# Kernel tuning notes

Hardware: AMD Instinct MI355X
Metric: run time of the kernel (lower is better)

Reference implementation:

```python
import jax, jax.numpy as jnp
import numpy as np

EMBED_DIM = 1024
NUM_HEADS = 16
HEAD_DIM = EMBED_DIM // NUM_HEADS


def setup_inputs() -> dict:
    key = jax.random.key(0)
    ks = jax.random.split(key, 9)
    B, S, E = 2, 2048, EMBED_DIM
    scale = 1.0 / np.sqrt(E)
    x = jax.random.normal(ks[0], (B, S, E), dtype=jnp.float32)
    Wq = jax.random.normal(ks[1], (E, E), dtype=jnp.float32) * scale
    bq = jax.random.normal(ks[2], (E,), dtype=jnp.float32) * 0.01
    Wk = jax.random.normal(ks[3], (E, E), dtype=jnp.float32) * scale
    bk = jax.random.normal(ks[4], (E,), dtype=jnp.float32) * 0.01
    Wv = jax.random.normal(ks[5], (E, E), dtype=jnp.float32) * scale
    bv = jax.random.normal(ks[6], (E,), dtype=jnp.float32) * 0.01
    Wo = jax.random.normal(ks[7], (E, E), dtype=jnp.float32) * scale
    bo = jax.random.normal(ks[8], (E,), dtype=jnp.float32) * 0.01
    return {"x": x, "Wq": Wq, "bq": bq, "Wk": Wk, "bk": bk,
            "Wv": Wv, "bv": bv, "Wo": Wo, "bo": bo}


def reference(x, Wq, bq, Wk, bk, Wv, bv, Wo, bo):
    B, S, E = x.shape
    H, D = NUM_HEADS, HEAD_DIM
    # projections (torch Linear: x @ W.T + b), reshape to (B, H, S, D)
    q = (x @ Wq.T + bq).reshape(B, S, H, D).transpose(0, 2, 1, 3)
    k = (x @ Wk.T + bk).reshape(B, S, H, D).transpose(0, 2, 1, 3)
    v = (x @ Wv.T + bv).reshape(B, S, H, D).transpose(0, 2, 1, 3)
    softmax_scale = 1.0 / np.sqrt(D)
    # (B, H, S, S) scores, causal mask, stable softmax
    scores = softmax_scale * jnp.einsum('bhsd,bhtd->bhst', q, k)
    causal = jnp.tril(jnp.ones((S, S), dtype=bool))  # True = keep
    scores = jnp.where(causal, scores, -jnp.inf)
    attn = jax.nn.softmax(scores, axis=-1)
    out = jnp.einsum('bhst,bhtd->bhsd', attn, v)  # (B, H, S, D)
    out = out.transpose(0, 2, 1, 3).reshape(B, S, E)
    return out @ Wo.T + bo
```

## Files before the change

kernel.cpp:

```cpp
#include <hip/hip_runtime.h>
#include <cstdint>
#include <cstddef>

#define SEQ   2048
#define BATCH 2
#define EMB   1024
#define NH    16
#define HD    64
#define MTOT  (BATCH * SEQ)
#define NX    (MTOT * EMB)
#define NW    (EMB * EMB)

typedef __bf16 bf16_t;
typedef __bf16 bf16x2 __attribute__((ext_vector_type(2)));
typedef __bf16 bf16x4 __attribute__((ext_vector_type(4)));
typedef __bf16 bf16x8 __attribute__((ext_vector_type(8)));
typedef float  f32x4  __attribute__((ext_vector_type(4)));
typedef float  f32x16 __attribute__((ext_vector_type(16)));

typedef __attribute__((address_space(1))) const void* as1cv;
typedef __attribute__((address_space(3))) void*       as3v;

__device__ __forceinline__ void async_cp16(const void* g, void* l) {
  __builtin_amdgcn_global_load_lds((as1cv)g, (as3v)l, 16, 0, 0);
}

__device__ __forceinline__ f32x4 mfma16(bf16x8 a, bf16x8 b, f32x4 c) {
  return __builtin_amdgcn_mfma_f32_16x16x32_bf16(a, b, c, 0, 0, 0);
}
__device__ __forceinline__ f32x16 mfma32(bf16x8 a, bf16x8 b, f32x16 c) {
  return __builtin_amdgcn_mfma_f32_32x32x16_bf16(a, b, c, 0, 0, 0);
}

__device__ __forceinline__ uint32_t pk2(float a, float b) {
  bf16x2 t; t[0] = (bf16_t)a; t[1] = (bf16_t)b;
  return __builtin_bit_cast(uint32_t, t);
}
__device__ __forceinline__ bf16x8 mk_frag(uint32_t x, uint32_t y,
                                          uint32_t z, uint32_t w) {
  uint4 u; u.x = x; u.y = y; u.z = z; u.w = w;
  return __builtin_bit_cast(bf16x8, u);
}

__global__ __launch_bounds__(256) void cvt_all(
    const float* __restrict__ x,  const float* __restrict__ wq,
    const float* __restrict__ wk, const float* __restrict__ wv,
    const float* __restrict__ wo,
    bf16_t* __restrict__ xb,  bf16_t* __restrict__ wqb,
    bf16_t* __restrict__ wkb, bf16_t* __restrict__ wvb,
    bf16_t* __restrict__ wob) {
  long e = ((long)blockIdx.x * 256 + threadIdx.x) * 4;
  const float* s; bf16_t* d; long off;
  if (e < NX) { s = x; d = xb; off = e; }
  else {
    long e2 = e - NX;
    int w = (int)(e2 >> 20);
    off = e2 & (NW - 1);
    s = (w == 0) ? wq : (w == 1) ? wk : (w == 2) ? wv : wo;
    d = (w == 0) ? wqb : (w == 1) ? wkb : (w == 2) ? wvb : wob;
  }
  float4 v = *(const float4*)(s + off);
  bf16x4 o;
  o[0] = (bf16_t)v.x; o[1] = (bf16_t)v.y; o[2] = (bf16_t)v.z; o[3] = (bf16_t)v.w;
  *(bf16x4*)(d + off) = o;
}

__global__ __launch_bounds__(256) void vtrans(const bf16_t* __restrict__ V,
                                              bf16_t* __restrict__ VT) {
  const int hb = blockIdx.x;
  const int sb = blockIdx.y;
  const int h = hb & 15, b = hb >> 4;
  const int t = threadIdx.x;
  __shared__ __align__(16) bf16_t Ts[64 * 72];
  const bf16_t* Vp = V + ((size_t)(b * SEQ + sb * 64)) * EMB + h * HD;
  const int sr = t >> 4, d0 = (t & 15) * 4;
#pragma unroll
  for (int i = 0; i < 4; ++i) {
    bf16x4 v = *(const bf16x4*)(Vp + (size_t)(sr + 16 * i) * EMB + d0);
    *(bf16x4*)&Ts[(sr + 16 * i) * 72 + d0] = v;
  }
  __syncthreads();
  const int d = t >> 2, tc = (t & 3) * 16;
  __align__(16) bf16_t out[16];
#pragma unroll
  for (int j = 0; j < 16; ++j) out[j] = Ts[(tc + j) * 72 + d];
  bf16_t* dst = VT + ((size_t)hb * HD + d) * SEQ + sb * 64 + tc;
  *(uint4*)(dst)     = *(uint4*)&out[0];
  *(uint4*)(dst + 8) = *(uint4*)&out[8];
}

template <typename OT>
__global__ __launch_bounds__(256) void gemm_bt3(
    const bf16_t* __restrict__ A,
    const bf16_t* __restrict__ W0, const bf16_t* __restrict__ W1,
    const bf16_t* __restrict__ W2,
    const float* __restrict__ b0, const float* __restrict__ b1,
    const float* __restrict__ b2,
    OT* __restrict__ C0, OT* __restrict__ C1, OT* __restrict__ C2) {
  constexpr int K = EMB, N = EMB, BK = 64;
  const int z = blockIdx.z;
  const bf16_t* B    = (z == 0) ? W0 : (z == 1) ? W1 : W2;
  const float*  bias = (z == 0) ? b0 : (z == 1) ? b1 : b2;
  OT*           C    = (z == 0) ? C0 : (z == 1) ? C1 : C2;

  __shared__ __align__(16) bf16_t As[128 * BK];
  __shared__ __align__(16) bf16_t Bs[64 * BK];

  const int tid  = threadIdx.x;
  const int lane = tid & 63;
  const int wave = tid >> 6;
  const int quad = lane >> 4;
  const int l16  = lane & 15;
  const int wm   = wave * 32;
  const int m0   = blockIdx.y * 128;
  const int n0   = blockIdx.x * 64;

  const int row0 = tid >> 3;
  const int slot = tid & 7;
  const bf16_t* gA[4];
  const bf16_t* gB[2];
#pragma unroll
  for (int i = 0; i < 4; ++i) {
    const int r = row0 + 32 * i;
    gA[i] = A + (size_t)(m0 + r) * K + (slot ^ (r & 7)) * 8;
  }
#pragma unroll
  for (int i = 0; i < 2; ++i) {
    const int r = row0 + 32 * i;
    gB[i] = B + (size_t)(n0 + r) * K + (slot ^ (r & 7)) * 8;
  }

  f32x4 acc[2][4] = {};
  const int sw = l16 & 7;

  for (int kk = 0; kk < K; kk += BK) {
#pragma unroll
    for (int i = 0; i < 4; ++i)
      async_cp16(gA[i] + kk, &As[(tid + 256 * i) * 8]);
#pragma unroll
    for (int i = 0; i < 2; ++i)
      async_cp16(gB[i] + kk, &Bs[(tid + 256 * i) * 8]);
    __syncthreads();

    bf16x8 af[2][2], bfr[2][4];
#pragma unroll
    for (int ks = 0; ks < 2; ++ks) {
      const int js = ((ks * 4 + quad) ^ sw) * 8;
#pragma unroll
      for (int i = 0; i < 2; ++i)
        af[ks][i] = *(const bf16x8*)&As[(wm + i * 16 + l16) * BK + js];
#pragma unroll
      for (int j = 0; j < 4; ++j)
        bfr[ks][j] = *(const bf16x8*)&Bs[(j * 16 + l16) * BK + js];
    }
#pragma unroll
    for (int ks = 0; ks < 2; ++ks)
#pragma unroll
      for (int i = 0; i < 2; ++i)
#pragma unroll
        for (int j = 0; j < 4; ++j)
          acc[i][j] = mfma16(af[ks][i], bfr[ks][j], acc[i][j]);
    __syncthreads();
  }

#pragma unroll
  for (int j = 0; j < 4; ++j) {
    const int col = n0 + j * 16 + l16;
    const float bv = bias[col];
#pragma unroll
    for (int i = 0; i < 2; ++i) {
      const int row = m0 + wm + i * 16 + quad * 4;
#pragma unroll
      for (int r = 0; r < 4; ++r) {
        C[(size_t)(row + r) * N + col] = (OT)(acc[i][j][r] + bv);
      }
    }
  }
}

__global__ __launch_bounds__(256, 3) void attn128(
    const bf16_t* __restrict__ Qg, const bf16_t* __restrict__ Kg,
    const bf16_t* __restrict__ VTg, bf16_t* __restrict__ Og) {
  const int hb  = blockIdx.x;
  const int y   = blockIdx.y;
  const int s   = (y < 8) ? (15 - y) : (y - 8);
  const int h   = hb & 15, b = hb >> 4;
  const int tid = threadIdx.x;
  const int lane = tid & 63, wave = tid >> 6;
  const int l31 = lane & 31, hi = lane >> 5;
  const bool h0 = (hi == 0);

  __shared__ __align__(16) bf16_t Ks[2][64 * 72];
  __shared__ __align__(16) bf16_t VsT[2][64 * 72];
  __shared__ __align__(16) bf16_t Qs[128 * 64];

  const size_t base = ((size_t)b * SEQ) * EMB + (size_t)h * HD;
  const bf16_t* Kp  = Kg + base;
  const bf16_t* VTp = VTg + (size_t)hb * HD * SEQ;

  const int kr0r = tid >> 3, kcol = (tid & 7) * 8;
  const int kr1r = kr0r + 32;
  const int lo0 = kr0r * 72 + kcol;
  const int lo1 = lo0 + 32 * 72;

  const int q0  = s * 128;
  const int nit = 2 * s + 2;
  const bf16_t* Qp = Qg + base + (size_t)q0 * EMB;

  uint4 kr0 = *(const uint4*)(Kp + (size_t)kr0r * EMB + kcol);
  uint4 kr1 = *(const uint4*)(Kp + (size_t)kr1r * EMB + kcol);
  uint4 vr0 = *(const uint4*)(VTp + (size_t)kr0r * SEQ + kcol);
  uint4 vr1 = *(const uint4*)(VTp + (size_t)kr1r * SEQ + kcol);

#pragma unroll
  for (int i = 0; i < 4; ++i) {
    const int c = tid + 256 * i;
    *(uint4*)&Qs[(c >> 3) * 64 + (c & 7) * 8] =
        *(const uint4*)(Qp + (size_t)(c >> 3) * EMB + (c & 7) * 8);
  }
  __syncthreads();

  bf16x8 qf[4];
#pragma unroll
  for (int kk = 0; kk < 4; ++kk)
    qf[kk] = *(const bf16x8*)&Qs[(32 * wave + l31) * 64 + kk * 16 + hi * 8];

  f32x16 acc_t0 = {}, acc_t1 = {};
  float lsum = 0.f;

  for (int it = 0; it < nit; ++it) {
    bf16_t* Kc = &Ks[it & 1][0];
    bf16_t* Vc = &VsT[it & 1][0];
    *(uint4*)&Kc[lo0] = kr0;
    *(uint4*)&Kc[lo1] = kr1;
    *(uint4*)&Vc[lo0] = vr0;
    *(uint4*)&Vc[lo1] = vr1;
    __syncthreads();

    if (it + 1 < nit) {
      const bf16_t* Kn  = Kp + (size_t)(it + 1) * 64 * EMB;
      const bf16_t* VTn = VTp + (it + 1) * 64;
      kr0 = *(const uint4*)(Kn + (size_t)kr0r * EMB + kcol);
      kr1 = *(const uint4*)(Kn + (size_t)kr1r * EMB + kcol);
      vr0 = *(const uint4*)(VTn + (size_t)kr0r * SEQ + kcol);
      vr1 = *(const uint4*)(VTn + (size_t)kr1r * SEQ + kcol);
    }

    const bool active = (64 * it <= q0 + 32 * wave + 31);
    if (active) {
      f32x16 s0 = {}, s1 = {};
#pragma unroll
      for (int kk = 0; kk < 4; ++kk) {
        const bf16x8 kf0 = *(const bf16x8*)&Kc[l31 * 72 + kk * 16 + hi * 8];
        const bf16x8 kf1 =
            *(const bf16x8*)&Kc[(32 + l31) * 72 + kk * 16 + hi * 8];
        s0 = mfma32(kf0, qf[kk], s0);
        s1 = mfma32(kf1, qf[kk], s1);
      }

      constexpr float SC2 = 0.18033688011112042f;
      if (it >= nit - 2) {
        const int qg = q0 + 32 * wave + l31;
        const int k0 = 64 * it + 4 * hi;
#pragma unroll
        for (int r = 0; r < 16; ++r) {
          const int key = k0 + (r & 3) + 8 * (r >> 2);
          float p0 = exp2f(__builtin_fmaf(s0[r], SC2, -8.f));
          float p1 = exp2f(__builtin_fmaf(s1[r], SC2, -8.f));
          if (key > qg) p0 = 0.f;
          if (key + 32 > qg) p1 = 0.f;
          s0[r] = p0; s1[r] = p1;
          lsum += p0 + p1;
        }
      } else {
#pragma unroll
        for (int r = 0; r < 16; ++r) {
          const float p0 = exp2f(__builtin_fmaf(s0[r], SC2, -8.f));
          const float p1 = exp2f(__builtin_fmaf(s1[r], SC2, -8.f));
          s0[r] = p0; s1[r] = p1;
          lsum += p0 + p1;
        }
      }

      bf16x8 pf[4];
#pragma unroll
      for (int kk = 0; kk < 4; ++kk) {
        const f32x16& g = (kk < 2) ? s0 : s1;
        const int bir = 8 * (kk & 1);
        const uint32_t PL0 = pk2(g[bir + 0], g[bir + 1]);
        const uint32_t PL1 = pk2(g[bir + 2], g[bir + 3]);
        const uint32_t PH0 = pk2(g[bir + 4], g[bir + 5]);
        const uint32_t PH1 = pk2(g[bir + 6], g[bir + 7]);
        const uint32_t XL0 = (uint32_t)__shfl_xor((int)PL0, 32, 64);
        const uint32_t XL1 = (uint32_t)__shfl_xor((int)PL1, 32, 64);
        const uint32_t XH0 = (uint32_t)__shfl_xor((int)PH0, 32, 64);
        const uint32_t XH1 = (uint32_t)__shfl_xor((int)PH1, 32, 64);
        pf[kk] = h0 ? mk_frag(PL0, PL1, XL0, XL1)
                    : mk_frag(XH0, XH1, PH0, PH1);
      }

#pragma unroll
      for (int kk = 0; kk < 4; ++kk) {
        const bf16x8 vf0 = *(const bf16x8*)&Vc[l31 * 72 + kk * 16 + hi * 8];
        const bf16x8 vf1 =
            *(const bf16x8*)&Vc[(32 + l31) * 72 + kk * 16 + hi * 8];
        acc_t0 = mfma32(vf0, pf[kk], acc_t0);
        acc_t1 = mfma32(vf1, pf[kk], acc_t1);
      }
    }
  }

  const float lt = lsum + __shfl_xor(lsum, 32, 64);
  const float inv = 1.f / lt;
  bf16_t* Ow = &Qs[(32 * wave) * 64];
#pragma unroll
  for (int a = 0; a < 4; ++a)
#pragma unroll
    for (int c = 0; c < 4; c += 2) {
      const int r = 4 * a + c;
      const int d = c + 8 * a + 4 * hi;
      *(uint32_t*)&Ow[l31 * 64 + d] =
          pk2(acc_t0[r] * inv, acc_t0[r + 1] * inv);
      *(uint32_t*)&Ow[l31 * 64 + d + 32] =
          pk2(acc_t1[r] * inv, acc_t1[r + 1] * inv);
    }
  bf16_t* Op = Og + base + (size_t)(q0 + 32 * wave) * EMB;
#pragma unroll
  for (int i = 0; i < 4; ++i) {
    const int id = lane + 64 * i;
    const int row = id >> 3, col8 = (id & 7) * 8;
    *(uint4*)(Op + (size_t)row * EMB + col8) =
        *(const uint4*)&Ow[row * 64 + col8];
  }
}

extern "C" void kernel_launch(void* const* d_in, const int* in_sizes, int n_in,
                              void* d_out, int out_size, void* d_ws,
                              size_t ws_size, hipStream_t stream) {
  const float* x  = (const float*)d_in[0];
  const float* Wq = (const float*)d_in[1];
  const float* bq = (const float*)d_in[2];
  const float* Wk = (const float*)d_in[3];
  const float* bk = (const float*)d_in[4];
  const float* Wv = (const float*)d_in[5];
  const float* bv = (const float*)d_in[6];
  const float* Wo = (const float*)d_in[7];
  const float* bo = (const float*)d_in[8];
  float* out = (float*)d_out;

  char* p = (char*)d_ws;
  bf16_t* xb  = (bf16_t*)p; p += (size_t)NX * 2;
  bf16_t* wqb = (bf16_t*)p; p += (size_t)NW * 2;
  bf16_t* wkb = (bf16_t*)p; p += (size_t)NW * 2;
  bf16_t* wvb = (bf16_t*)p; p += (size_t)NW * 2;
  bf16_t* wob = (bf16_t*)p; p += (size_t)NW * 2;
  bf16_t* qb  = (bf16_t*)p; p += (size_t)NX * 2;
  bf16_t* kb  = (bf16_t*)p; p += (size_t)NX * 2;
  bf16_t* vb  = (bf16_t*)p; p += (size_t)NX * 2;
  bf16_t* ab  = (bf16_t*)p; p += (size_t)NX * 2;
  bf16_t* vtb = xb;

  const int ntot = NX + 4 * NW;
  cvt_all<<<dim3(ntot / 4 / 256), 256, 0, stream>>>(
      x, Wq, Wk, Wv, Wo, xb, wqb, wkb, wvb, wob);

  gemm_bt3<bf16_t><<<dim3(EMB / 64, MTOT / 128, 3), 256, 0, stream>>>(
      xb, wqb, wkb, wvb, bq, bk, bv, qb, kb, vb);

  vtrans<<<dim3(BATCH * NH, SEQ / 64), 256, 0, stream>>>(vb, vtb);

  attn128<<<dim3(BATCH * NH, SEQ / 128), 256, 0, stream>>>(qb, kb, vtb, ab);

  gemm_bt3<float><<<dim3(EMB / 64, MTOT / 128, 1), 256, 0, stream>>>(
      ab, wob, wob, wob, bo, bo, bo, out, out, out);
}
```

Measured before the change: 191.6 us.

## Fuse QKV projection into one wide GEMM with 32x32 MFMA tiles

```diff
diff --git a/kernel.cpp b/kernel.cpp
--- a/kernel.cpp
+++ b/kernel.cpp
@@ -10,6 +10,7 @@
 #define MTOT  (BATCH * SEQ)
 #define NX    (MTOT * EMB)
 #define NW    (EMB * EMB)
+#define QS    3072
 
 typedef __bf16 bf16_t;
 typedef __bf16 bf16x2 __attribute__((ext_vector_type(2)));
@@ -25,9 +26,6 @@
   __builtin_amdgcn_global_load_lds((as1cv)g, (as3v)l, 16, 0, 0);
 }
 
-__device__ __forceinline__ f32x4 mfma16(bf16x8 a, bf16x8 b, f32x4 c) {
-  return __builtin_amdgcn_mfma_f32_16x16x32_bf16(a, b, c, 0, 0, 0);
-}
 __device__ __forceinline__ f32x16 mfma32(bf16x8 a, bf16x8 b, f32x16 c) {
   return __builtin_amdgcn_mfma_f32_32x32x16_bf16(a, b, c, 0, 0, 0);
 }
@@ -65,18 +63,18 @@
   *(bf16x4*)(d + off) = o;
 }
 
-__global__ __launch_bounds__(256) void vtrans(const bf16_t* __restrict__ V,
+__global__ __launch_bounds__(256) void vtrans(const bf16_t* __restrict__ QKV,
                                               bf16_t* __restrict__ VT) {
   const int hb = blockIdx.x;
   const int sb = blockIdx.y;
   const int h = hb & 15, b = hb >> 4;
   const int t = threadIdx.x;
   __shared__ __align__(16) bf16_t Ts[64 * 72];
-  const bf16_t* Vp = V + ((size_t)(b * SEQ + sb * 64)) * EMB + h * HD;
+  const bf16_t* Vp = QKV + ((size_t)(b * SEQ + sb * 64)) * QS + 2048 + h * HD;
   const int sr = t >> 4, d0 = (t & 15) * 4;
 #pragma unroll
   for (int i = 0; i < 4; ++i) {
-    bf16x4 v = *(const bf16x4*)(Vp + (size_t)(sr + 16 * i) * EMB + d0);
+    bf16x4 v = *(const bf16x4*)(Vp + (size_t)(sr + 16 * i) * QS + d0);
     *(bf16x4*)&Ts[(sr + 16 * i) * 72 + d0] = v;
   }
   __syncthreads();
@@ -89,98 +87,85 @@
   *(uint4*)(dst + 8) = *(uint4*)&out[8];
 }
 
-template <typename OT>
-__global__ __launch_bounds__(256) void gemm_bt3(
-    const bf16_t* __restrict__ A,
-    const bf16_t* __restrict__ W0, const bf16_t* __restrict__ W1,
-    const bf16_t* __restrict__ W2,
+template <typename OT, int BN, int CS>
+__global__ __launch_bounds__(256) void gemm_f(
+    const bf16_t* __restrict__ A, const bf16_t* __restrict__ Bw,
     const float* __restrict__ b0, const float* __restrict__ b1,
-    const float* __restrict__ b2,
-    OT* __restrict__ C0, OT* __restrict__ C1, OT* __restrict__ C2) {
-  constexpr int K = EMB, N = EMB, BK = 64;
-  const int z = blockIdx.z;
-  const bf16_t* B    = (z == 0) ? W0 : (z == 1) ? W1 : W2;
-  const float*  bias = (z == 0) ? b0 : (z == 1) ? b1 : b2;
-  OT*           C    = (z == 0) ? C0 : (z == 1) ? C1 : C2;
-
+    const float* __restrict__ b2, OT* __restrict__ C) {
+  constexpr int K = EMB, BK = 64;
   __shared__ __align__(16) bf16_t As[128 * BK];
-  __shared__ __align__(16) bf16_t Bs[64 * BK];
+  __shared__ __align__(16) bf16_t Bs[BN * BK];
 
   const int tid  = threadIdx.x;
   const int lane = tid & 63;
   const int wave = tid >> 6;
-  const int quad = lane >> 4;
-  const int l16  = lane & 15;
-  const int wm   = wave * 32;
+  const int l31  = lane & 31;
+  const int hi   = lane >> 5;
+  const int wm   = (wave >> 1) * 64;
+  const int wn   = (wave & 1) * (BN / 2);
   const int m0   = blockIdx.y * 128;
-  const int n0   = blockIdx.x * 64;
-
-  const int row0 = tid >> 3;
-  const int slot = tid & 7;
+  const int n0   = blockIdx.x * BN;
+
+  const float* bias = (n0 < 1024) ? b0 : ((n0 < 2048) ? b1 : b2);
+
+  const int row0 = tid >> 3, slot = tid & 7;
   const bf16_t* gA[4];
-  const bf16_t* gB[2];
-#pragma unroll
-  for (int i = 0; i < 4; ++i) {
-    const int r = row0 + 32 * i;
-    gA[i] = A + (size_t)(m0 + r) * K + (slot ^ (r & 7)) * 8;
-  }
-#pragma unroll
-  for (int i = 0; i < 2; ++i) {
-    const int r = row0 + 32 * i;
-    gB[i] = B + (size_t)(n0 + r) * K + (slot ^ (r & 7)) * 8;
-  }
-
-  f32x4 acc[2][4] = {};
-  const int sw = l16 & 7;
+  const bf16_t* gB[BN / 32];
+#pragma unroll
+  for (int i = 0; i < 4; ++i)
+    gA[i] = A + (size_t)(m0 + row0 + 32 * i) * K + (slot ^ (row0 & 7)) * 8;
+#pragma unroll
+  for (int i = 0; i < BN / 32; ++i)
+    gB[i] = Bw + (size_t)(n0 + row0 + 32 * i) * K + (slot ^ (row0 & 7)) * 8;
+
+  f32x16 acc[2][BN / 64] = {};
+  const int sw = l31 & 7;
 
   for (int kk = 0; kk < K; kk += BK) {
 #pragma unroll
     for (int i = 0; i < 4; ++i)
       async_cp16(gA[i] + kk, &As[(tid + 256 * i) * 8]);
 #pragma unroll
-    for (int i = 0; i < 2; ++i)
+    for (int i = 0; i < BN / 32; ++i)
       async_cp16(gB[i] + kk, &Bs[(tid + 256 * i) * 8]);
     __syncthreads();
 
-    bf16x8 af[2][2], bfr[2][4];
-#pragma unroll
-    for (int ks = 0; ks < 2; ++ks) {
-      const int js = ((ks * 4 + quad) ^ sw) * 8;
+#pragma unroll
+    for (int ks = 0; ks < 4; ++ks) {
+      const int js = ((ks * 2 + hi) ^ sw) * 8;
+      bf16x8 af[2], bfr[BN / 64];
 #pragma unroll
       for (int i = 0; i < 2; ++i)
-        af[ks][i] = *(const bf16x8*)&As[(wm + i * 16 + l16) * BK + js];
-#pragma unroll
-      for (int j = 0; j < 4; ++j)
-        bfr[ks][j] = *(const bf16x8*)&Bs[(j * 16 + l16) * BK + js];
-    }
-#pragma unroll
-    for (int ks = 0; ks < 2; ++ks)
+        af[i] = *(const bf16x8*)&As[(wm + i * 32 + l31) * BK + js];
+#pragma unroll
+      for (int j = 0; j < BN / 64; ++j)
+        bfr[j] = *(const bf16x8*)&Bs[(wn + j * 32 + l31) * BK + js];
 #pragma unroll
       for (int i = 0; i < 2; ++i)
 #pragma unroll
-        for (int j = 0; j < 4; ++j)
-          acc[i][j] = mfma16(af[ks][i], bfr[ks][j], acc[i][j]);
+        for (int j = 0; j < BN / 64; ++j)
+          acc[i][j] = mfma32(af[i], bfr[j], acc[i][j]);
+    }
     __syncthreads();
   }
 
 #pragma unroll
-  for (int j = 0; j < 4; ++j) {
-    const int col = n0 + j * 16 + l16;
-    const float bv = bias[col];
-#pragma unroll
-    for (int i = 0; i < 2; ++i) {
-      const int row = m0 + wm + i * 16 + quad * 4;
-#pragma unroll
-      for (int r = 0; r < 4; ++r) {
-        C[(size_t)(row + r) * N + col] = (OT)(acc[i][j][r] + bv);
-      }
-    }
-  }
+  for (int i = 0; i < 2; ++i)
+#pragma unroll
+    for (int j = 0; j < BN / 64; ++j) {
+      const int col = n0 + wn + j * 32 + l31;
+      const float bv = bias[col & 1023];
+#pragma unroll
+      for (int r = 0; r < 16; ++r) {
+        const int row = m0 + wm + i * 32 + (r & 3) + 8 * (r >> 2) + 4 * hi;
+        C[(size_t)row * CS + col] = (OT)(acc[i][j][r] + bv);
+      }
+    }
 }
 
 __global__ __launch_bounds__(256, 3) void attn128(
-    const bf16_t* __restrict__ Qg, const bf16_t* __restrict__ Kg,
-    const bf16_t* __restrict__ VTg, bf16_t* __restrict__ Og) {
+    const bf16_t* __restrict__ QKVg, const bf16_t* __restrict__ VTg,
+    bf16_t* __restrict__ Og) {
   const int hb  = blockIdx.x;
   const int y   = blockIdx.y;
   const int s   = (y < 8) ? (15 - y) : (y - 8);
@@ -194,8 +179,9 @@
   __shared__ __align__(16) bf16_t VsT[2][64 * 72];
   __shared__ __align__(16) bf16_t Qs[128 * 64];
 
-  const size_t base = ((size_t)b * SEQ) * EMB + (size_t)h * HD;
-  const bf16_t* Kp  = Kg + base;
+  const size_t base = ((size_t)b * SEQ) * QS + (size_t)h * HD;
+  const bf16_t* Qb  = QKVg + base;
+  const bf16_t* Kp  = QKVg + base + 1024;
   const bf16_t* VTp = VTg + (size_t)hb * HD * SEQ;
 
   const int kr0r = tid >> 3, kcol = (tid & 7) * 8;
@@ -205,10 +191,10 @@
 
   const int q0  = s * 128;
   const int nit = 2 * s + 2;
-  const bf16_t* Qp = Qg + base + (size_t)q0 * EMB;
-
-  uint4 kr0 = *(const uint4*)(Kp + (size_t)kr0r * EMB + kcol);
-  uint4 kr1 = *(const uint4*)(Kp + (size_t)kr1r * EMB + kcol);
+  const bf16_t* Qp = Qb + (size_t)q0 * QS;
+
+  uint4 kr0 = *(const uint4*)(Kp + (size_t)kr0r * QS + kcol);
+  uint4 kr1 = *(const uint4*)(Kp + (size_t)kr1r * QS + kcol);
   uint4 vr0 = *(const uint4*)(VTp + (size_t)kr0r * SEQ + kcol);
   uint4 vr1 = *(const uint4*)(VTp + (size_t)kr1r * SEQ + kcol);
 
@@ -216,7 +202,7 @@
   for (int i = 0; i < 4; ++i) {
     const int c = tid + 256 * i;
     *(uint4*)&Qs[(c >> 3) * 64 + (c & 7) * 8] =
-        *(const uint4*)(Qp + (size_t)(c >> 3) * EMB + (c & 7) * 8);
+        *(const uint4*)(Qp + (size_t)(c >> 3) * QS + (c & 7) * 8);
   }
   __syncthreads();
 
@@ -238,10 +224,10 @@
     __syncthreads();
 
     if (it + 1 < nit) {
-      const bf16_t* Kn  = Kp + (size_t)(it + 1) * 64 * EMB;
+      const bf16_t* Kn  = Kp + (size_t)(it + 1) * 64 * QS;
       const bf16_t* VTn = VTp + (it + 1) * 64;
-      kr0 = *(const uint4*)(Kn + (size_t)kr0r * EMB + kcol);
-      kr1 = *(const uint4*)(Kn + (size_t)kr1r * EMB + kcol);
+      kr0 = *(const uint4*)(Kn + (size_t)kr0r * QS + kcol);
+      kr1 = *(const uint4*)(Kn + (size_t)kr1r * QS + kcol);
       vr0 = *(const uint4*)(VTn + (size_t)kr0r * SEQ + kcol);
       vr1 = *(const uint4*)(VTn + (size_t)kr1r * SEQ + kcol);
     }
@@ -324,7 +310,7 @@
       *(uint32_t*)&Ow[l31 * 64 + d + 32] =
           pk2(acc_t1[r] * inv, acc_t1[r + 1] * inv);
     }
-  bf16_t* Op = Og + base + (size_t)(q0 + 32 * wave) * EMB;
+  bf16_t* Op = Og + ((size_t)b * SEQ + q0 + 32 * wave) * EMB + (size_t)h * HD;
 #pragma unroll
   for (int i = 0; i < 4; ++i) {
     const int id = lane + 64 * i;
@@ -349,28 +335,26 @@
   float* out = (float*)d_out;
 
   char* p = (char*)d_ws;
-  bf16_t* xb  = (bf16_t*)p; p += (size_t)NX * 2;
-  bf16_t* wqb = (bf16_t*)p; p += (size_t)NW * 2;
-  bf16_t* wkb = (bf16_t*)p; p += (size_t)NW * 2;
-  bf16_t* wvb = (bf16_t*)p; p += (size_t)NW * 2;
-  bf16_t* wob = (bf16_t*)p; p += (size_t)NW * 2;
-  bf16_t* qb  = (bf16_t*)p; p += (size_t)NX * 2;
-  bf16_t* kb  = (bf16_t*)p; p += (size_t)NX * 2;
-  bf16_t* vb  = (bf16_t*)p; p += (size_t)NX * 2;
-  bf16_t* ab  = (bf16_t*)p; p += (size_t)NX * 2;
-  bf16_t* vtb = xb;
+  bf16_t* xb   = (bf16_t*)p; p += (size_t)NX * 2;
+  bf16_t* wqb  = (bf16_t*)p; p += (size_t)NW * 2;
+  bf16_t* wkb  = (bf16_t*)p; p += (size_t)NW * 2;
+  bf16_t* wvb  = (bf16_t*)p; p += (size_t)NW * 2;
+  bf16_t* wob  = (bf16_t*)p; p += (size_t)NW * 2;
+  bf16_t* qkvb = (bf16_t*)p; p += (size_t)NX * 3 * 2;
+  bf16_t* ab   = (bf16_t*)p; p += (size_t)NX * 2;
+  bf16_t* vtb  = xb;
 
   const int ntot = NX + 4 * NW;
   cvt_all<<<dim3(ntot / 4 / 256), 256, 0, stream>>>(
       x, Wq, Wk, Wv, Wo, xb, wqb, wkb, wvb, wob);
 
-  gemm_bt3<bf16_t><<<dim3(EMB / 64, MTOT / 128, 3), 256, 0, stream>>>(
-      xb, wqb, wkb, wvb, bq, bk, bv, qb, kb, vb);
-
-  vtrans<<<dim3(BATCH * NH, SEQ / 64), 256, 0, stream>>>(vb, vtb);
-
-  attn128<<<dim3(BATCH * NH, SEQ / 128), 256, 0, stream>>>(qb, kb, vtb, ab);
-
-  gemm_bt3<float><<<dim3(EMB / 64, MTOT / 128, 1), 256, 0, stream>>>(
-      ab, wob, wob, wob, bo, bo, bo, out, out, out);
-}
+  gemm_f<bf16_t, 128, QS><<<dim3(QS / 128, MTOT / 128), 256, 0, stream>>>(
+      xb, wqb, bq, bk, bv, qkvb);
+
+  vtrans<<<dim3(BATCH * NH, SEQ / 64), 256, 0, stream>>>(qkvb, vtb);
+
+  attn128<<<dim3(BATCH * NH, SEQ / 128), 256, 0, stream>>>(qkvb, vtb, ab);
+
+  gemm_f<float, 64, EMB><<<dim3(EMB / 64, MTOT / 128), 256, 0, stream>>>(
+      ab, wob, bo, bo, bo, out);
+}
```

After: 187.4 us. 2.2% less time.
